# Performance work log

Hardware: AMD Instinct MI355X
Metric: run time of the kernel (lower is better)

## Reference

```python
import jax, jax.numpy as jnp
import numpy as np

N_E = 512
E_DIM = 128
LEGACY = 0.2
B, T = 64, 1024


def setup_inputs() -> dict:
    key = jax.random.key(0)
    k1, k2 = jax.random.split(key, 2)
    key_soft = jax.random.normal(k1, (B, T, E_DIM), dtype=jnp.float32)
    emb_weight = jax.random.uniform(k2, (N_E + 1, E_DIM), dtype=jnp.float32,
                                    minval=-1.0 / N_E, maxval=1.0 / N_E)
    zero_ts_mask = jnp.zeros((B,), dtype=jnp.bool_)
    return {"key_soft": key_soft, "emb_weight": emb_weight, "zero_ts_mask": zero_ts_mask}


def _neighbor_indices(d, zero_ts_mask, n_e):
    # d: [B, T, n_e+1] (no grad needed; only used for int index selection)
    ind0 = jnp.clip(jnp.argmin(d[:, 0, :], axis=1), 0, n_e - 1)
    ind0 = jnp.where(zero_ts_mask, 0, ind0)

    def step(ind, d_t):  # ind: [B], d_t: [B, n_e+1]
        d_here = jnp.take_along_axis(d_t, ind[:, None], axis=1)[:, 0]
        ind_next = jnp.clip(ind + 1, 0, n_e - 1)
        d_next = jnp.take_along_axis(d_t, ind_next[:, None], axis=1)[:, 0]
        ind_new = jnp.where(d_here <= d_next, ind, ind_next)
        return ind_new, ind_new

    _, rest = jax.lax.scan(step, ind0, jnp.swapaxes(d[:, 1:, :], 0, 1))  # [T-1, B]
    return jnp.concatenate([ind0[None, :], rest], axis=0).T  # [B, T]


def reference(key_soft, emb_weight, zero_ts_mask):
    sg = jax.lax.stop_gradient
    n_e = emb_weight.shape[0] - 1
    b, t, e_dim = key_soft.shape

    # squared-distance matrix: [B, T, n_e+1]
    d = (jnp.sum(key_soft ** 2, axis=-1, keepdims=True)
         + jnp.sum(emb_weight ** 2, axis=1)
         - 2.0 * jnp.einsum('btd,nd->btn', key_soft, emb_weight))
    d_ng = sg(d)

    min_indices = jnp.argmin(d_ng, axis=-1)                 # [B, T] (over full n_e+1)
    enc = _neighbor_indices(d_ng, zero_ts_mask, n_e)        # [B, T]

    key_hard_here = emb_weight[enc]                                  # [B, T, D]
    key_hard_next = emb_weight[jnp.clip(enc + 1, 0, n_e - 1)]        # [B, T, D]
    key_min = emb_weight[min_indices]                                # [B, T, D]

    def vq_loss(kh):
        return (jnp.sum((sg(key_soft) - kh) ** 2, axis=-1)
                + jnp.sum((key_soft - sg(kh)) ** 2, axis=-1) * LEGACY)

    loss_here_base = vq_loss(key_hard_here)
    loss_next_base = vq_loss(key_hard_next)

    energy = (jnp.sum((sg(key_soft) - key_hard_next) ** 2, axis=-1)
              - jnp.sum((sg(key_soft) - key_hard_here) ** 2, axis=-1)
              + (jnp.sum((key_soft - sg(key_hard_next)) ** 2, axis=-1)
                 - jnp.sum((key_soft - sg(key_hard_here)) ** 2, axis=-1)) * LEGACY)

    change = (enc[:, 1:] - enc[:, :-1]) != 0
    same_hard_mask = jnp.where(change, 0.0, 1.0)
    energy_change = (energy[:, 1:] - energy[:, :-1]) * same_hard_mask
    loss_energy_descent = jnp.maximum(energy_change + 1e-06 / n_e,
                                      jnp.zeros_like(energy_change)).mean()
    energy_mean = energy.mean()

    loss_min_indices = vq_loss(key_min)
    loss_min_here = jnp.where(loss_min_indices < loss_here_base, loss_min_indices, 0.0)
    loss_min_next = jnp.where(loss_min_indices < loss_next_base, loss_min_indices, 0.0)

    loss_here = loss_here_base - loss_next_base - loss_min_here
    loss_next = loss_next_base - loss_here_base - loss_min_next

    key_hard = key_soft + sg(key_hard_here - key_soft)  # straight-through

    v = jnp.max(jnp.max(enc, axis=1) - jnp.min(enc, axis=1))
    return (key_hard, enc, v, loss_here, loss_next, energy_mean, loss_energy_descent)
```

## Files before the change

kernel.cpp:

```cpp
#include <hip/hip_runtime.h>
#include <cfloat>
#include <cstdint>

#define B_  64
#define T_  1024
#define D_  128
#define NE  512
#define P_  (B_*T_)

#define O_KH   0
#define O_ENC  (P_*D_)
#define O_V    (O_ENC + P_)
#define O_LH   (O_V + 1)
#define O_LN   (O_LH + P_)
#define O_EM   (O_LN + P_)
#define O_LED  (O_EM + 1)

typedef __attribute__((ext_vector_type(8))) short bf16x8;
typedef __attribute__((ext_vector_type(4))) float floatx4;
typedef unsigned long long u64;

__device__ __forceinline__ void pack8(const float4& a, const float4& b,
                                      uint4& h, uint4& l)
{
    float v[8] = {a.x,a.y,a.z,a.w,b.x,b.y,b.z,b.w};
    unsigned hw[4], lw[4];
    #pragma unroll
    for (int e = 0; e < 4; e++) {
        const unsigned ua = __float_as_uint(v[2*e]);
        const unsigned ub = __float_as_uint(v[2*e+1]);
        const float fa = __uint_as_float(ua & 0xffff0000u);
        const float fb = __uint_as_float(ub & 0xffff0000u);
        const unsigned da = __float_as_uint(v[2*e]   - fa);
        const unsigned db = __float_as_uint(v[2*e+1] - fb);
        hw[e] = (ub & 0xffff0000u) | (ua >> 16);
        lw[e] = (db & 0xffff0000u) | (da >> 16);
    }
    h = make_uint4(hw[0],hw[1],hw[2],hw[3]);
    l = make_uint4(lw[0],lw[1],lw[2],lw[3]);
}

__device__ __forceinline__ u64 shflx64(u64 v, int d)
{
    const int lo = __shfl_xor((int)(unsigned)(v & 0xffffffffULL), d);
    const int hi = __shfl_xor((int)(unsigned)(v >> 32), d);
    return ((u64)(unsigned)hi << 32) | (unsigned)lo;
}

__global__ __launch_bounds__(256) void kF(const float* __restrict__ emb,
                                          unsigned short* __restrict__ ehi,
                                          unsigned short* __restrict__ elo,
                                          float* __restrict__ sq)
{
    const int t = blockIdx.x * 256 + threadIdx.x;
    const int n = t >> 2, kst = t & 3;
    const float4* src = (const float4*)(emb + (size_t)n * D_ + kst * 32);
    float ss = 0.f;
    #pragma unroll
    for (int g = 0; g < 4; g++) {
        const float4 a = src[2*g], b = src[2*g+1];
        ss += a.x*a.x + a.y*a.y + a.z*a.z + a.w*a.w
            + b.x*b.x + b.y*b.y + b.z*b.z + b.w*b.w;
        uint4 h, l;
        pack8(a, b, h, l);
        const int f = ((n >> 4) * 4 + kst) * 4 + g;
        *(uint4*)(ehi + (size_t)f*128 + (size_t)(n & 15)*8) = h;
        *(uint4*)(elo + (size_t)f*128 + (size_t)(n & 15)*8) = l;
    }
    ss += __shfl_xor(ss, 1);
    ss += __shfl_xor(ss, 2);
    if (kst == 0) sq[n] = ss;
}

__global__ __launch_bounds__(256) void kA(const float* __restrict__ ks,
                                          const float* __restrict__ sq,
                                          const unsigned short* __restrict__ ehi,
                                          const unsigned short* __restrict__ elo,
                                          u64* __restrict__ bits,
                                          float* __restrict__ sfirst,
                                          float* __restrict__ slast,
                                          float* __restrict__ minv,
                                          int* __restrict__ mini)
{
    __shared__ unsigned short Bhi[16*64*8];
    __shared__ unsigned short Blo[16*64*8];

    const int tid  = threadIdx.x;
    const int lane = tid & 63;
    const int wv   = tid >> 6;
    const int m    = lane & 15;
    const int q    = lane >> 4;
    const int p0   = (blockIdx.x >> 1) * 64;
    const int ch   = (blockIdx.x & 1) * 4 + wv;
    const int nb   = ch * 64;

    {
        const int row = tid >> 2;
        const int kh  = tid & 3;
        const float4* src = (const float4*)(ks + (size_t)(p0 + row) * D_ + kh * 32);
        #pragma unroll
        for (int g = 0; g < 4; g++) {
            uint4 h, l;
            pack8(src[2*g], src[2*g+1], h, l);
            const int kq = kh*4 + g;
            *(uint4*)&Bhi[(kq*64 + row)*8] = h;
            *(uint4*)&Blo[(kq*64 + row)*8] = l;
        }
    }
    __syncthreads();

    floatx4 acc[4][4];
    #pragma unroll
    for (int i = 0; i < 4; i++)
        #pragma unroll
        for (int j = 0; j < 4; j++)
            #pragma unroll
            for (int r = 0; r < 4; r++) acc[i][j][r] = 0.f;

    #pragma unroll 1
    for (int kst = 0; kst < 4; kst++) {
        bf16x8 ah[4], al[4], bh[4], bl[4];
        #pragma unroll
        for (int i = 0; i < 4; i++) {
            const int f = ((ch*4 + i) * 4 + kst) * 4 + q;
            const int off = f*128 + m*8;
            ah[i] = *(const bf16x8*)(ehi + off);
            al[i] = *(const bf16x8*)(elo + off);
        }
        const int kq = kst*4 + q;
        #pragma unroll
        for (int j = 0; j < 4; j++) {
            bh[j] = *(const bf16x8*)&Bhi[(kq*64 + j*16 + m)*8];
            bl[j] = *(const bf16x8*)&Blo[(kq*64 + j*16 + m)*8];
        }
        #pragma unroll
        for (int i = 0; i < 4; i++)
            #pragma unroll
            for (int j = 0; j < 4; j++)
                acc[i][j] = __builtin_amdgcn_mfma_f32_16x16x32_bf16(ah[i], bh[j], acc[i][j], 0, 0, 0);
        #pragma unroll
        for (int i = 0; i < 4; i++)
            #pragma unroll
            for (int j = 0; j < 4; j++)
                acc[i][j] = __builtin_amdgcn_mfma_f32_16x16x32_bf16(ah[i], bl[j], acc[i][j], 0, 0, 0);
        #pragma unroll
        for (int i = 0; i < 4; i++)
            #pragma unroll
            for (int j = 0; j < 4; j++)
                acc[i][j] = __builtin_amdgcn_mfma_f32_16x16x32_bf16(al[i], bh[j], acc[i][j], 0, 0, 0);
    }

    float sa[4][4];
    #pragma unroll
    for (int i = 0; i < 4; i++) {
        const float4 s4 = *(const float4*)(sq + nb + i*16 + q*4);
        sa[i][0]=s4.x; sa[i][1]=s4.y; sa[i][2]=s4.z; sa[i][3]=s4.w;
    }
    #pragma unroll
    for (int j = 0; j < 4; j++) {
        float S[4][4];
        #pragma unroll
        for (int i = 0; i < 4; i++)
            #pragma unroll
            for (int r = 0; r < 4; r++)
                S[i][r] = fmaf(-2.f, acc[i][j][r], sa[i][r]);

        float nq[4], ni[4];
        #pragma unroll
        for (int i = 0; i < 4; i++) nq[i] = __shfl_down(S[i][0], 16);
        #pragma unroll
        for (int i = 0; i < 3; i++) ni[i] = __shfl(S[i+1][0], m);
        ni[3] = 0.f;

        u64 w = 0;
        #pragma unroll
        for (int i = 0; i < 4; i++) {
            #pragma unroll
            for (int r = 0; r < 3; r++)
                w |= (u64)(S[i][r] <= S[i][r+1]) << (16*i + 4*q + r);
            if (!(i == 3 && q == 3)) {
                const float nxt = (q < 3) ? nq[i] : ni[i];
                w |= (u64)(S[i][3] <= nxt) << (16*i + 4*q + 3);
            }
        }
        if (ch == 7 && q == 3) w |= 1ULL << 63;
        w |= shflx64(w, 16);
        w |= shflx64(w, 32);

        float mv = S[0][0]; int mi_ = nb + q*4;
        #pragma unroll
        for (int i = 0; i < 4; i++)
            #pragma unroll
            for (int r = 0; r < 4; r++) {
                if (i == 0 && r == 0) continue;
                const int nid = nb + 16*i + 4*q + r;
                if (S[i][r] < mv) { mv = S[i][r]; mi_ = nid; }
            }
        #pragma unroll
        for (int d = 16; d <= 32; d <<= 1) {
            const float v2 = __shfl_xor(mv, d);
            const int   i2 = __shfl_xor(mi_, d);
            if (v2 < mv || (v2 == mv && i2 < mi_)) { mv = v2; mi_ = i2; }
        }

        const size_t pg = (size_t)(p0 + j*16 + m);
        if (q == 0) {
            bits  [pg*8 + ch] = w;
            sfirst[pg*8 + ch] = S[0][0];
            minv  [pg*8 + ch] = mv;
            mini  [pg*8 + ch] = mi_;
        }
        if (q == 3) slast[pg*8 + ch] = S[3][3];
    }
}

struct KBwin { u64 W[8]; float F[8]; float L[8]; };

__global__ __launch_bounds__(64) void kB(const float* __restrict__ ks,
                                         const float* __restrict__ emb,
                                         const unsigned char* __restrict__ mask,
                                         const u64* __restrict__ bits,
                                         const float* __restrict__ sfirst,
                                         const float* __restrict__ slast,
                                         const float* __restrict__ minv,
                                         const int* __restrict__ mini,
                                         int* __restrict__ enci,
                                         float* __restrict__ out)
{
    const int b    = blockIdx.x;
    const int lane = threadIdx.x;
    const size_t p0 = (size_t)b * T_;

    const float2 e = ((const float2*)(emb + (size_t)512*D_))[lane];
    const float2 k = ((const float2*)(ks  + p0*D_))[lane];
    float s5 = e.x*(e.x - 2.f*k.x) + e.y*(e.y - 2.f*k.y);
    #pragma unroll
    for (int m = 32; m >= 1; m >>= 1) s5 += __shfl_xor(s5, m);

    float mv; int mi;
    if (lane < 8)       { mv = minv[p0*8 + lane]; mi = mini[p0*8 + lane]; }
    else if (lane == 8) { mv = s5; mi = 512; }
    else                { mv = FLT_MAX; mi = 0x7fffffff; }
    #pragma unroll
    for (int m = 32; m >= 1; m >>= 1) {
        float v2 = __shfl_xor(mv, m);
        int   i2 = __shfl_xor(mi, m);
        if (v2 < mv || (v2 == mv && i2 < mi)) { mv = v2; mi = i2; }
    }
    int cur = (mi < NE) ? mi : NE - 1;
    if (mask[b]) cur = 0;
    if (lane == 0) { enci[p0] = cur; out[O_ENC + p0] = (float)cur; }

    KBwin wa, wb;

    auto loadwin = [&](KBwin& d, int t0) {
        const int t = t0 + lane;
        if (t < T_) {
            const ulonglong2* bp = (const ulonglong2*)(bits + (p0 + t)*8);
            const ulonglong2 w01 = bp[0], w23 = bp[1], w45 = bp[2], w67 = bp[3];
            d.W[0]=w01.x; d.W[1]=w01.y; d.W[2]=w23.x; d.W[3]=w23.y;
            d.W[4]=w45.x; d.W[5]=w45.y; d.W[6]=w67.x; d.W[7]=w67.y;
            const float4* fp = (const float4*)(sfirst + (p0 + t)*8);
            const float4 f0 = fp[0], f1 = fp[1];
            d.F[0]=f0.x; d.F[1]=f0.y; d.F[2]=f0.z; d.F[3]=f0.w;
            d.F[4]=f1.x; d.F[5]=f1.y; d.F[6]=f1.z; d.F[7]=f1.w;
            const float4* lp = (const float4*)(slast + (p0 + t)*8);
            const float4 l0 = lp[0], l1 = lp[1];
            d.L[0]=l0.x; d.L[1]=l0.y; d.L[2]=l0.z; d.L[3]=l0.w;
            d.L[4]=l1.x; d.L[5]=l1.y; d.L[6]=l1.z; d.L[7]=l1.w;
        } else {
            #pragma unroll
            for (int c = 0; c < 8; c++) { d.W[c] = ~0ULL; d.F[c] = 1.f; d.L[c] = 0.f; }
        }
    };

    auto scanwin = [&](KBwin& d, int t0) {
        #pragma unroll
        for (int c = 0; c < 7; c++)
            d.W[c] |= (u64)(d.L[c] <= d.F[c+1]) << 63;

        const int w0   = cur >> 6;
        const int off0 = cur & 63;
        u64 a = d.W[0];
        #pragma unroll
        for (int c = 1; c < 8; c++) a = (w0 == c) ? d.W[c] : a;
        u64 bn = ~0ULL;
        #pragma unroll
        for (int c = 1; c < 8; c++) bn = (w0 == c-1) ? d.W[c] : bn;
        const u64 u = (off0 == 0) ? a : ((a >> off0) | (bn << (64 - off0)));

        const unsigned ulo = (unsigned)u;
        const unsigned uhi = (unsigned)(u >> 32);
        int doff = 0;
        int myenc = cur;
        #pragma unroll
        for (int j = 0; j < 64; j++) {
            const unsigned slo = (unsigned)__builtin_amdgcn_readlane((int)ulo, j);
            const unsigned shi = (unsigned)__builtin_amdgcn_readlane((int)uhi, j);
            const u64 word = ((u64)shi << 32) | slo;
            const int bit = (int)((word >> doff) & 1ULL);
            doff += 1 - bit;
            if (lane == j) myenc = cur + doff;
        }
        cur += doff;
        const int t = t0 + lane;
        if (t < T_) {
            enci[p0 + t] = myenc;
            out[O_ENC + p0 + t] = (float)myenc;
        }
    };

    loadwin(wa, 1);
    #pragma unroll 1
    for (int wp = 0; wp < 8; wp++) {
        const int t0a = 1 + wp*128;
        loadwin(wb, t0a + 64);
        scanwin(wa, t0a);
        if (wp < 7) loadwin(wa, t0a + 128);
        scanwin(wb, t0a + 64);
    }
}

__global__ __launch_bounds__(256) void kC(const float* __restrict__ ks,
                                          const float* __restrict__ emb,
                                          const int* __restrict__ enci,
                                          const float* __restrict__ minv,
                                          const int* __restrict__ mini,
                                          float* __restrict__ out,
                                          float* __restrict__ energy)
{
    const int lane = threadIdx.x & 63;
    const size_t p = (size_t)blockIdx.x * 4 + (threadIdx.x >> 6);

    const float2 k  = ((const float2*)(ks + p*D_))[lane];
    const int eh = enci[p];
    const int en = (eh + 1 < NE) ? eh + 1 : NE - 1;
    const float2 Eh = ((const float2*)(emb + (size_t)eh*D_))[lane];
    const float2 En = ((const float2*)(emb + (size_t)en*D_))[lane];
    const float2 E5 = ((const float2*)(emb + (size_t)512*D_))[lane];

    float ph  = Eh.x*(Eh.x - 2.f*k.x) + Eh.y*(Eh.y - 2.f*k.y);
    float pn  = En.x*(En.x - 2.f*k.x) + En.y*(En.y - 2.f*k.y);
    float p5  = E5.x*(E5.x - 2.f*k.x) + E5.y*(E5.y - 2.f*k.y);
    float sqk = k.x*k.x + k.y*k.y;
    #pragma unroll
    for (int m = 32; m >= 1; m >>= 1) {
        ph  += __shfl_xor(ph, m);
        pn  += __shfl_xor(pn, m);
        p5  += __shfl_xor(p5, m);
        sqk += __shfl_xor(sqk, m);
    }

    float mv; int mi;
    if (lane < 8)       { mv = minv[p*8 + lane]; mi = mini[p*8 + lane]; }
    else if (lane == 8) { mv = p5; mi = 512; }
    else                { mv = FLT_MAX; mi = 0x7fffffff; }
    #pragma unroll
    for (int m = 32; m >= 1; m >>= 1) {
        float v2 = __shfl_xor(mv, m);
        int   i2 = __shfl_xor(mi, m);
        if (v2 < mv || (v2 == mv && i2 < mi)) { mv = v2; mi = i2; }
    }

    const float2 Em = ((const float2*)(emb + (size_t)mi*D_))[lane];
    float pm = Em.x*(Em.x - 2.f*k.x) + Em.y*(Em.y - 2.f*k.y);
    #pragma unroll
    for (int m = 32; m >= 1; m >>= 1) pm += __shfl_xor(pm, m);

    const float lh = 1.2f * (sqk + ph);
    const float ln = 1.2f * (sqk + pn);
    const float lm = 1.2f * (sqk + pm);
    const float lossh = lh - ln - ((pm < ph) ? lm : 0.f);
    const float lossn = ln - lh - ((pm < pn) ? lm : 0.f);

    float2 kh;
    kh.x = k.x + (Eh.x - k.x);
    kh.y = k.y + (Eh.y - k.y);
    ((float2*)(out + p*D_))[lane] = kh;

    if (lane == 0) {
        out[O_LH + p] = lossh;
        out[O_LN + p] = lossn;
        energy[p] = 1.2f * (pn - ph);
    }
}

__global__ __launch_bounds__(256) void kD1(const float* __restrict__ energy,
                                           const int* __restrict__ enci,
                                           double2* __restrict__ part)
{
    __shared__ double sA[256], sB[256];
    const int p = blockIdx.x * 256 + threadIdx.x;
    const float e = energy[p];
    double se = (double)e;
    double sl = 0.0;
    if ((p & (T_-1)) < T_-1) {
        const float ec = (enci[p+1] == enci[p]) ? (energy[p+1] - e) : 0.f;
        sl = (double)fmaxf(ec + (float)(1e-6/512.0), 0.f);
    }
    sA[threadIdx.x] = se; sB[threadIdx.x] = sl;
    __syncthreads();
    for (int s = 128; s >= 1; s >>= 1) {
        if (threadIdx.x < (unsigned)s) {
            sA[threadIdx.x] += sA[threadIdx.x+s];
            sB[threadIdx.x] += sB[threadIdx.x+s];
        }
        __syncthreads();
    }
    if (threadIdx.x == 0) { part[blockIdx.x] = make_double2(sA[0], sB[0]); }
}

__global__ __launch_bounds__(256) void kD2(const double2* __restrict__ part,
                                           const int* __restrict__ enci,
                                           float* __restrict__ out)
{
    __shared__ double sA[256], sB[256];
    const double2 pv = part[threadIdx.x];
    sA[threadIdx.x] = pv.x; sB[threadIdx.x] = pv.y;
    __syncthreads();
    for (int s = 128; s >= 1; s >>= 1) {
        if (threadIdx.x < (unsigned)s) {
            sA[threadIdx.x] += sA[threadIdx.x+s];
            sB[threadIdx.x] += sB[threadIdx.x+s];
        }
        __syncthreads();
    }
    if (threadIdx.x < 64) {
        int v = enci[(size_t)threadIdx.x*T_ + T_-1] - enci[(size_t)threadIdx.x*T_];
        #pragma unroll
        for (int m = 32; m >= 1; m >>= 1) {
            const int v2 = __shfl_xor(v, m);
            v = (v2 > v) ? v2 : v;
        }
        if (threadIdx.x == 0) {
            out[O_V]   = (float)v;
            out[O_EM]  = (float)(sA[0] / (double)P_);
            out[O_LED] = (float)(sB[0] / (double)(B_*(T_-1)));
        }
    }
}

extern "C" void kernel_launch(void* const* d_in, const int* in_sizes, int n_in,
                              void* d_out, int out_size, void* d_ws, size_t ws_size,
                              hipStream_t stream)
{
    const float* ks  = (const float*)d_in[0];
    const float* emb = (const float*)d_in[1];
    const unsigned char* mask = (const unsigned char*)d_in[2];

    float* out = (float*)d_out;
    char* w = (char*)d_ws;
    u64*   bits   = (u64*)  (w);
    float* sfirst = (float*)(w + (size_t) 4*1024*1024);
    float* slast  = (float*)(w + (size_t) 6*1024*1024);
    float* minv   = (float*)(w + (size_t) 8*1024*1024);
    int*   mini   = (int*)  (w + (size_t)10*1024*1024);
    int*   enci   = (int*)  (w + (size_t)12*1024*1024);
    float* energy = (float*)(w + (size_t)12*1024*1024 + 256*1024);
    float* sq     = (float*)(w + (size_t)12*1024*1024 + 512*1024);
    double2* part = (double2*)(w + (size_t)12*1024*1024 + 516*1024);
    unsigned short* ehi = (unsigned short*)(w + (size_t)12*1024*1024 + 640*1024);
    unsigned short* elo = (unsigned short*)(w + (size_t)12*1024*1024 + 768*1024);

    kF <<<8,    256, 0, stream>>>(emb, ehi, elo, sq);
    kA <<<2048, 256, 0, stream>>>(ks, sq, ehi, elo, bits, sfirst, slast, minv, mini);
    kB <<<B_,   64,  0, stream>>>(ks, emb, mask, bits, sfirst, slast, minv, mini, enci, out);
    kC <<<P_/4, 256, 0, stream>>>(ks, emb, enci, minv, mini, out, energy);
    kD1<<<256,  256, 0, stream>>>(energy, enci, part);
    kD2<<<1,    256, 0, stream>>>(part, enci, out);
}
```

Before: 197.2 us.

## Prepack key bf16 splits once, pack argmin keys, and restructure per-point loss kernel

```diff
diff --git a/kernel.cpp b/kernel.cpp
--- a/kernel.cpp
+++ b/kernel.cpp
@@ -47,6 +47,12 @@
     return ((u64)(unsigned)hi << 32) | (unsigned)lo;
 }
 
+__device__ __forceinline__ unsigned sortkey(float f)
+{
+    const unsigned b = __float_as_uint(f);
+    return b ^ (unsigned)(((int)b >> 31) | (int)0x80000000);
+}
+
 __global__ __launch_bounds__(256) void kF(const float* __restrict__ emb,
                                           unsigned short* __restrict__ ehi,
                                           unsigned short* __restrict__ elo,
@@ -72,42 +78,44 @@
     if (kst == 0) sq[n] = ss;
 }
 
-__global__ __launch_bounds__(256) void kA(const float* __restrict__ ks,
-                                          const float* __restrict__ sq,
+__global__ __launch_bounds__(256) void kG(const float* __restrict__ ks,
+                                          unsigned short* __restrict__ khi,
+                                          unsigned short* __restrict__ klo)
+{
+    const int pt  = blockIdx.x;
+    const int kh  = threadIdx.x >> 6;
+    const int row = threadIdx.x & 63;
+    const float4* src = (const float4*)(ks + ((size_t)pt*64 + row)*D_ + kh*32);
+    #pragma unroll
+    for (int g = 0; g < 4; g++) {
+        uint4 h, l;
+        pack8(src[2*g], src[2*g+1], h, l);
+        const size_t o = ((size_t)(pt*16 + kh*4 + g)*64 + row)*8;
+        *(uint4*)(khi + o) = h;
+        *(uint4*)(klo + o) = l;
+    }
+}
+
+__global__ __launch_bounds__(256) void kA(const float* __restrict__ sq,
                                           const unsigned short* __restrict__ ehi,
                                           const unsigned short* __restrict__ elo,
+                                          const unsigned short* __restrict__ khi,
+                                          const unsigned short* __restrict__ klo,
                                           u64* __restrict__ bits,
                                           float* __restrict__ sfirst,
                                           float* __restrict__ slast,
-                                          float* __restrict__ minv,
-                                          int* __restrict__ mini)
-{
-    __shared__ unsigned short Bhi[16*64*8];
-    __shared__ unsigned short Blo[16*64*8];
-
+                                          unsigned* __restrict__ mins,
+                                          unsigned short* __restrict__ mini16)
+{
     const int tid  = threadIdx.x;
     const int lane = tid & 63;
     const int wv   = tid >> 6;
     const int m    = lane & 15;
     const int q    = lane >> 4;
-    const int p0   = (blockIdx.x >> 1) * 64;
+    const int pt   = blockIdx.x >> 1;
+    const int p0   = pt * 64;
     const int ch   = (blockIdx.x & 1) * 4 + wv;
     const int nb   = ch * 64;
-
-    {
-        const int row = tid >> 2;
-        const int kh  = tid & 3;
-        const float4* src = (const float4*)(ks + (size_t)(p0 + row) * D_ + kh * 32);
-        #pragma unroll
-        for (int g = 0; g < 4; g++) {
-            uint4 h, l;
-            pack8(src[2*g], src[2*g+1], h, l);
-            const int kq = kh*4 + g;
-            *(uint4*)&Bhi[(kq*64 + row)*8] = h;
-            *(uint4*)&Blo[(kq*64 + row)*8] = l;
-        }
-    }
-    __syncthreads();
 
     floatx4 acc[4][4];
     #pragma unroll
@@ -122,16 +130,15 @@
         bf16x8 ah[4], al[4], bh[4], bl[4];
         #pragma unroll
         for (int i = 0; i < 4; i++) {
-            const int f = ((ch*4 + i) * 4 + kst) * 4 + q;
-            const int off = f*128 + m*8;
+            const int off = (((ch*4 + i) * 4 + kst) * 4 + q) * 128 + m*8;
             ah[i] = *(const bf16x8*)(ehi + off);
             al[i] = *(const bf16x8*)(elo + off);
         }
-        const int kq = kst*4 + q;
         #pragma unroll
         for (int j = 0; j < 4; j++) {
-            bh[j] = *(const bf16x8*)&Bhi[(kq*64 + j*16 + m)*8];
-            bl[j] = *(const bf16x8*)&Blo[(kq*64 + j*16 + m)*8];
+            const int off = ((pt*16 + kst*4 + q) * 64 + j*16 + m) * 8;
+            bh[j] = *(const bf16x8*)(khi + off);
+            bl[j] = *(const bf16x8*)(klo + off);
         }
         #pragma unroll
         for (int i = 0; i < 4; i++)
@@ -207,8 +214,8 @@
         if (q == 0) {
             bits  [pg*8 + ch] = w;
             sfirst[pg*8 + ch] = S[0][0];
-            minv  [pg*8 + ch] = mv;
-            mini  [pg*8 + ch] = mi_;
+            mins  [pg*8 + ch] = sortkey(mv);
+            mini16[pg*8 + ch] = (unsigned short)mi_;
         }
         if (q == 3) slast[pg*8 + ch] = S[3][3];
     }
@@ -222,8 +229,8 @@
                                          const u64* __restrict__ bits,
                                          const float* __restrict__ sfirst,
                                          const float* __restrict__ slast,
-                                         const float* __restrict__ minv,
-                                         const int* __restrict__ mini,
+                                         const unsigned* __restrict__ mins,
+                                         const unsigned short* __restrict__ mini16,
                                          int* __restrict__ enci,
                                          float* __restrict__ out)
 {
@@ -237,16 +244,15 @@
     #pragma unroll
     for (int m = 32; m >= 1; m >>= 1) s5 += __shfl_xor(s5, m);
 
-    float mv; int mi;
-    if (lane < 8)       { mv = minv[p0*8 + lane]; mi = mini[p0*8 + lane]; }
-    else if (lane == 8) { mv = s5; mi = 512; }
-    else                { mv = FLT_MAX; mi = 0x7fffffff; }
-    #pragma unroll
-    for (int m = 32; m >= 1; m >>= 1) {
-        float v2 = __shfl_xor(mv, m);
-        int   i2 = __shfl_xor(mi, m);
-        if (v2 < mv || (v2 == mv && i2 < mi)) { mv = v2; mi = i2; }
-    }
+    u64 kk = ~0ULL;
+    if (lane < 8)       kk = ((u64)mins[p0*8 + lane] << 32) | (u64)mini16[p0*8 + lane];
+    else if (lane == 8) kk = ((u64)sortkey(s5) << 32) | 512ULL;
+    #pragma unroll
+    for (int d = 1; d <= 8; d <<= 1) {
+        const u64 o = shflx64(kk, d);
+        kk = (o < kk) ? o : kk;
+    }
+    const int mi = __shfl((int)(unsigned)(kk & 0xffffffffULL), 0);
     int cur = (mi < NE) ? mi : NE - 1;
     if (mask[b]) cur = 0;
     if (lane == 0) { enci[p0] = cur; out[O_ENC + p0] = (float)cur; }
@@ -324,63 +330,85 @@
 __global__ __launch_bounds__(256) void kC(const float* __restrict__ ks,
                                           const float* __restrict__ emb,
                                           const int* __restrict__ enci,
-                                          const float* __restrict__ minv,
-                                          const int* __restrict__ mini,
+                                          const unsigned* __restrict__ mins,
+                                          const unsigned short* __restrict__ mini16,
                                           float* __restrict__ out,
                                           float* __restrict__ energy)
 {
     const int lane = threadIdx.x & 63;
     const size_t p = (size_t)blockIdx.x * 4 + (threadIdx.x >> 6);
-
-    const float2 k  = ((const float2*)(ks + p*D_))[lane];
+    const int q  = lane >> 4;
+    const int qm = lane & 15;
+
     const int eh = enci[p];
     const int en = (eh + 1 < NE) ? eh + 1 : NE - 1;
-    const float2 Eh = ((const float2*)(emb + (size_t)eh*D_))[lane];
-    const float2 En = ((const float2*)(emb + (size_t)en*D_))[lane];
-    const float2 E5 = ((const float2*)(emb + (size_t)512*D_))[lane];
-
-    float ph  = Eh.x*(Eh.x - 2.f*k.x) + Eh.y*(Eh.y - 2.f*k.y);
-    float pn  = En.x*(En.x - 2.f*k.x) + En.y*(En.y - 2.f*k.y);
-    float p5  = E5.x*(E5.x - 2.f*k.x) + E5.y*(E5.y - 2.f*k.y);
-    float sqk = k.x*k.x + k.y*k.y;
-    #pragma unroll
-    for (int m = 32; m >= 1; m >>= 1) {
-        ph  += __shfl_xor(ph, m);
-        pn  += __shfl_xor(pn, m);
-        p5  += __shfl_xor(p5, m);
-        sqk += __shfl_xor(sqk, m);
-    }
-
-    float mv; int mi;
-    if (lane < 8)       { mv = minv[p*8 + lane]; mi = mini[p*8 + lane]; }
-    else if (lane == 8) { mv = p5; mi = 512; }
-    else                { mv = FLT_MAX; mi = 0x7fffffff; }
-    #pragma unroll
-    for (int m = 32; m >= 1; m >>= 1) {
-        float v2 = __shfl_xor(mv, m);
-        int   i2 = __shfl_xor(mi, m);
-        if (v2 < mv || (v2 == mv && i2 < mi)) { mv = v2; mi = i2; }
-    }
-
-    const float2 Em = ((const float2*)(emb + (size_t)mi*D_))[lane];
-    float pm = Em.x*(Em.x - 2.f*k.x) + Em.y*(Em.y - 2.f*k.y);
-    #pragma unroll
-    for (int m = 32; m >= 1; m >>= 1) pm += __shfl_xor(pm, m);
-
-    const float lh = 1.2f * (sqk + ph);
-    const float ln = 1.2f * (sqk + pn);
-    const float lm = 1.2f * (sqk + pm);
-    const float lossh = lh - ln - ((pm < ph) ? lm : 0.f);
-    const float lossn = ln - lh - ((pm < pn) ? lm : 0.f);
-
-    float2 kh;
-    kh.x = k.x + (Eh.x - k.x);
-    kh.y = k.y + (Eh.y - k.y);
-    ((float2*)(out + p*D_))[lane] = kh;
+    const int row = (q == 0) ? eh : ((q == 1) ? en : 512);
+
+    const float4* ksp = (const float4*)(ks + p*D_);
+    const float4 k1 = ksp[qm*2], k2 = ksp[qm*2 + 1];
+    const float4* ep = (const float4*)(emb + (size_t)row*D_);
+    const float4 e1 = ep[qm*2], e2 = ep[qm*2 + 1];
+
+    float d;
+    if (q == 3) {
+        d = k1.x*k1.x + k1.y*k1.y + k1.z*k1.z + k1.w*k1.w
+          + k2.x*k2.x + k2.y*k2.y + k2.z*k2.z + k2.w*k2.w;
+    } else {
+        d = e1.x*(e1.x - 2.f*k1.x) + e1.y*(e1.y - 2.f*k1.y)
+          + e1.z*(e1.z - 2.f*k1.z) + e1.w*(e1.w - 2.f*k1.w)
+          + e2.x*(e2.x - 2.f*k2.x) + e2.y*(e2.y - 2.f*k2.y)
+          + e2.z*(e2.z - 2.f*k2.z) + e2.w*(e2.w - 2.f*k2.w);
+    }
+    #pragma unroll
+    for (int s = 1; s <= 8; s <<= 1) d += __shfl_xor(d, s);
+
+    const float ph  = __shfl(d, 0);
+    const float pn  = __shfl(d, 16);
+    const float p5  = __shfl(d, 32);
+    const float sqk = __shfl(d, 48);
+
+    u64 kk = ~0ULL;
+    if (lane < 8)       kk = ((u64)mins[p*8 + lane] << 32) | (u64)mini16[p*8 + lane];
+    else if (lane == 8) kk = ((u64)sortkey(p5) << 32) | 512ULL;
+    #pragma unroll
+    for (int s = 1; s <= 8; s <<= 1) {
+        const u64 o = shflx64(kk, s);
+        kk = (o < kk) ? o : kk;
+    }
+    const int mi = __shfl((int)(unsigned)(kk & 0xffffffffULL), 0);
+
+    float pm;
+    if (mi == eh)      pm = ph;
+    else if (mi == en) pm = pn;
+    else if (mi == 512) pm = p5;
+    else {
+        const float4* mp = (const float4*)(emb + (size_t)mi*D_);
+        const float4 m1 = mp[qm*2], m2 = mp[qm*2 + 1];
+        float dm = m1.x*(m1.x - 2.f*k1.x) + m1.y*(m1.y - 2.f*k1.y)
+                 + m1.z*(m1.z - 2.f*k1.z) + m1.w*(m1.w - 2.f*k1.w)
+                 + m2.x*(m2.x - 2.f*k2.x) + m2.y*(m2.y - 2.f*k2.y)
+                 + m2.z*(m2.z - 2.f*k2.z) + m2.w*(m2.w - 2.f*k2.w);
+        #pragma unroll
+        for (int s = 1; s <= 8; s <<= 1) dm += __shfl_xor(dm, s);
+        pm = __shfl(dm, 0);
+    }
+
+    if (q == 0) {
+        float4 o1, o2;
+        o1.x = k1.x + (e1.x - k1.x); o1.y = k1.y + (e1.y - k1.y);
+        o1.z = k1.z + (e1.z - k1.z); o1.w = k1.w + (e1.w - k1.w);
+        o2.x = k2.x + (e2.x - k2.x); o2.y = k2.y + (e2.y - k2.y);
+        o2.z = k2.z + (e2.z - k2.z); o2.w = k2.w + (e2.w - k2.w);
+        ((float4*)(out + p*D_))[qm*2]     = o1;
+        ((float4*)(out + p*D_))[qm*2 + 1] = o2;
+    }
 
     if (lane == 0) {
-        out[O_LH + p] = lossh;
-        out[O_LN + p] = lossn;
+        const float lh = 1.2f * (sqk + ph);
+        const float ln = 1.2f * (sqk + pn);
+        const float lm = 1.2f * (sqk + pm);
+        out[O_LH + p] = lh - ln - ((pm < ph) ? lm : 0.f);
+        out[O_LN + p] = ln - lh - ((pm < pn) ? lm : 0.f);
         energy[p] = 1.2f * (pn - ph);
     }
 }
@@ -450,22 +478,25 @@
 
     float* out = (float*)d_out;
     char* w = (char*)d_ws;
-    u64*   bits   = (u64*)  (w);
-    float* sfirst = (float*)(w + (size_t) 4*1024*1024);
-    float* slast  = (float*)(w + (size_t) 6*1024*1024);
-    float* minv   = (float*)(w + (size_t) 8*1024*1024);
-    int*   mini   = (int*)  (w + (size_t)10*1024*1024);
-    int*   enci   = (int*)  (w + (size_t)12*1024*1024);
-    float* energy = (float*)(w + (size_t)12*1024*1024 + 256*1024);
-    float* sq     = (float*)(w + (size_t)12*1024*1024 + 512*1024);
-    double2* part = (double2*)(w + (size_t)12*1024*1024 + 516*1024);
-    unsigned short* ehi = (unsigned short*)(w + (size_t)12*1024*1024 + 640*1024);
-    unsigned short* elo = (unsigned short*)(w + (size_t)12*1024*1024 + 768*1024);
+    u64*      bits   = (u64*)     (w);
+    float*    sfirst = (float*)   (w + (size_t) 4*1024*1024);
+    float*    slast  = (float*)   (w + (size_t) 6*1024*1024);
+    unsigned* mins   = (unsigned*)(w + (size_t) 8*1024*1024);
+    unsigned short* mini16 = (unsigned short*)(w + (size_t)10*1024*1024);
+    int*      enci   = (int*)     (w + (size_t)11*1024*1024);
+    float*    energy = (float*)   (w + (size_t)11*1024*1024 + 256*1024);
+    float*    sq     = (float*)   (w + (size_t)11*1024*1024 + 512*1024);
+    double2*  part   = (double2*) (w + (size_t)11*1024*1024 + 516*1024);
+    unsigned short* ehi = (unsigned short*)(w + (size_t)11*1024*1024 + 640*1024);
+    unsigned short* elo = (unsigned short*)(w + (size_t)11*1024*1024 + 768*1024);
+    unsigned short* khi = (unsigned short*)d_out;
+    unsigned short* klo = (unsigned short*)((char*)d_out + (size_t)16*1024*1024);
 
     kF <<<8,    256, 0, stream>>>(emb, ehi, elo, sq);
-    kA <<<2048, 256, 0, stream>>>(ks, sq, ehi, elo, bits, sfirst, slast, minv, mini);
-    kB <<<B_,   64,  0, stream>>>(ks, emb, mask, bits, sfirst, slast, minv, mini, enci, out);
-    kC <<<P_/4, 256, 0, stream>>>(ks, emb, enci, minv, mini, out, energy);
+    kG <<<1024, 256, 0, stream>>>(ks, khi, klo);
+    kA <<<2048, 256, 0, stream>>>(sq, ehi, elo, khi, klo, bits, sfirst, slast, mins, mini16);
+    kB <<<B_,   64,  0, stream>>>(ks, emb, mask, bits, sfirst, slast, mins, mini16, enci, out);
+    kC <<<P_/4, 256, 0, stream>>>(ks, emb, enci, mins, mini16, out, energy);
     kD1<<<256,  256, 0, stream>>>(energy, enci, part);
     kD2<<<1,    256, 0, stream>>>(part, enci, out);
 }
```

New measurement: 200.2 us. About the same (+1.6%).
